# Performance work log

Measured on AMD Instinct MI355X. Metric: run time of the kernel, lower is better.

Reference implementation:

```python
import jax, jax.numpy as jnp
import numpy as np
import math

B, N, C, H = 32, 512, 768, 12
HD = C // H
KEEP_RATE = 0.7
SCALE = HD ** -0.5
BOUNDARY = math.ceil(KEEP_RATE * (N - 1))  # 358


def setup_inputs() -> dict:
    key = jax.random.key(0)
    k1, k2, k3, k4 = jax.random.split(key, 4)
    x = jax.random.normal(k1, (B, N, C), jnp.float32) * 0.02
    # prefix (left-aligned) key-padding mask: valid length per sample in [N//4, N]
    lengths = jax.random.randint(k2, (B,), N // 4, N + 1)
    key_mask = (jnp.arange(N)[None, :] < lengths[:, None])  # [B, N]
    attn_mask = jnp.broadcast_to(key_mask[:, None, :], (B, N, N)).astype(jnp.int32)
    w_qkv = jax.random.normal(k3, (C, 3 * C), jnp.float32) * (C ** -0.5)
    w_proj = jax.random.normal(k4, (C, C), jnp.float32) * (C ** -0.5)
    b_proj = jnp.zeros((C,), jnp.float32)
    return {"x": x, "attn_mask": attn_mask, "w_qkv": w_qkv, "w_proj": w_proj, "b_proj": b_proj}


def reference(x, attn_mask, w_qkv, w_proj, b_proj):
    # qkv projection and head split: [B,N,3C] -> [3,B,H,N,HD]
    qkv = (x @ w_qkv).reshape(B, N, 3, H, HD).transpose(2, 0, 3, 1, 4)
    q, k, v = qkv[0], qkv[1], qkv[2]
    attn = jnp.einsum('bhqd,bhkd->bhqk', q, k) * SCALE          # [B,H,N,N]
    mask4 = attn_mask[:, None, :, :]                            # broadcast over heads
    attn = jnp.where(mask4 == 0, jnp.float32(-1e9), attn)
    attn = jax.nn.softmax(attn, axis=-1)
    out = jnp.einsum('bhqk,bhkd->bhqd', attn, v)                # [B,H,N,HD]
    out = out.transpose(0, 2, 1, 3).reshape(B, N, C)
    out = out @ w_proj + b_proj

    # per-sample top-k token pruning based on CLS attention (keep_rate < 1)
    key_row = attn_mask[:, 0, 1:]                               # [B, N-1] key padding row
    cls_mean = attn[:, :, 0, 1:].mean(axis=1)                   # mean over heads, [B, N-1]
    valid = key_row != 0
    scores = jnp.where(valid, cls_mean, -jnp.inf)
    valid_count = valid.sum(axis=1)                             # [B]
    left = jnp.ceil(valid_count.astype(jnp.float32) * KEEP_RATE).astype(jnp.int32)
    _, top_idx = jax.lax.top_k(scores, BOUNDARY)                # sorted desc, [B, BOUNDARY]
    pos = jnp.arange(BOUNDARY)[None, :]
    # slots beyond per-sample left_tokens are padded with 1e9 (matches torch cat padding)
    idx = jnp.where(pos < left[:, None], top_idx.astype(jnp.float32), jnp.float32(1e9))
    index = jnp.broadcast_to(idx[:, :, None], (B, BOUNDARY, C))
    return (out, index, idx, BOUNDARY)
```

## Files before the change

### kernel.cpp

```cpp
#include <hip/hip_runtime.h>
#include <hip/hip_bf16.h>

#define Bb 32
#define Nn 512
#define Cc 768
#define Hh 12
#define HDd 64
#define BND 358
#define QS 0.18033688f

typedef unsigned short u16;
typedef unsigned int u32;
typedef __attribute__((ext_vector_type(8))) short bf16x8;
typedef __attribute__((ext_vector_type(4))) float f32x4;
typedef __attribute__((ext_vector_type(16))) float f32x16;
typedef __attribute__((ext_vector_type(4))) int i32x4;

__device__ __forceinline__ f32x4 MFMA16(bf16x8 a, bf16x8 b, f32x4 c) {
  return __builtin_amdgcn_mfma_f32_16x16x32_bf16(a, b, c, 0, 0, 0);
}
__device__ __forceinline__ f32x16 MFMA32(bf16x8 a, bf16x8 b, f32x16 c) {
  return __builtin_amdgcn_mfma_f32_32x32x16_bf16(a, b, c, 0, 0, 0);
}

__device__ __forceinline__ float fexp2(float x) { return __builtin_amdgcn_exp2f(x); }

__device__ __forceinline__ u32 f2bf(float f) {
  u32 u = __builtin_bit_cast(u32, f);
  return (u + 0x7fffu + ((u >> 16) & 1u)) >> 16;
}
__device__ __forceinline__ u32 packbf2(float a, float b) { return f2bf(a) | (f2bf(b) << 16); }
__device__ __forceinline__ u32 cvtpk2(float a, float b) {
  float2 f2 = {a, b};
  __hip_bfloat162 h = __float22bfloat162_rn(f2);
  u32 r;
  __builtin_memcpy(&r, &h, 4);
  return r;
}
__device__ __forceinline__ float bf2f(u16 h) { return __builtin_bit_cast(float, (u32)h << 16); }

__device__ __forceinline__ void async_copy16(void* lds, const void* g) {
  __builtin_amdgcn_global_load_lds((const __attribute__((address_space(1))) void*)g,
                                   (__attribute__((address_space(3))) void*)lds, 16, 0, 0);
}


__global__ __launch_bounds__(256) void k_convx(const float* __restrict__ x, u16* __restrict__ xb) {
  int gid = blockIdx.x * 256 + threadIdx.x;
  if (gid >= (Bb * Nn * Cc) / 4) return;
  float4 v = *(const float4*)&x[gid * 4];
  u32 p0 = packbf2(v.x, v.y), p1 = packbf2(v.z, v.w);
  uint2 st = {p0, p1};
  *(uint2*)&xb[gid * 4] = st;
}

__global__ __launch_bounds__(256) void k_transpose(const float* __restrict__ src, u16* __restrict__ dst,
                                                   int R, int Ccols) {
  __shared__ float tbuf[32][33];
  int c0 = blockIdx.x * 32, r0 = blockIdx.y * 32;
  int lx = threadIdx.x & 31, ly = threadIdx.x >> 5;
  #pragma unroll
  for (int rr = ly; rr < 32; rr += 8) tbuf[rr][lx] = src[(long)(r0 + rr) * Ccols + c0 + lx];
  __syncthreads();
  #pragma unroll
  for (int cc = ly; cc < 32; cc += 8) dst[(long)(c0 + cc) * R + r0 + lx] = (u16)f2bf(tbuf[lx][cc]);
}

__global__ __launch_bounds__(256) void k_lens(const int* __restrict__ mask, int* __restrict__ lens) {
  int b = blockIdx.x, t = threadIdx.x;
  __shared__ int red[256];
  red[t] = mask[(long)b * Nn * Nn + t] + mask[(long)b * Nn * Nn + t + 256];
  __syncthreads();
  for (int s = 128; s > 0; s >>= 1) {
    if (t < s) red[t] += red[t + s];
    __syncthreads();
  }
  if (t == 0) lens[b] = red[0];
}

__global__ __launch_bounds__(64) void k_order(const int* __restrict__ lens, int* __restrict__ ord) {
  __shared__ int ls[32];
  int t = threadIdx.x;
  if (t < 32) ls[t] = lens[t];
  __syncthreads();
  if (t < 32) {
    int mylen = ls[t];
    int rank = 0;
    #pragma unroll
    for (int j = 0; j < 32; ++j) {
      int lj = ls[j];
      rank += (lj > mylen || (lj == mylen && j < t)) ? 1 : 0;
    }
    int s = (rank < 16) ? (2 * rank) : (2 * (31 - rank) + 1);
    ord[s] = t;
  }
}

template <int MODE, int SWAP>
__global__ __launch_bounds__(256) void k_gemm2(const u16* __restrict__ A, const u16* __restrict__ Bt,
                                               int nb0, u16* __restrict__ Qo, u16* __restrict__ Ko,
                                               u16* __restrict__ Vto, float* __restrict__ Co,
                                               const float* __restrict__ bias) {
  __shared__ u16 As[2][128 * 64];
  __shared__ u16 Bs[2][128 * 64];
  int m0 = blockIdx.x * 128;
  int nb = nb0 + blockIdx.y * 128;
  int t = threadIdx.x, lane = t & 63, wave = t >> 6;
  int wr = wave >> 1, wc = wave & 1;
  int qlane = lane & 15, g = lane >> 4;
  f32x4 acc[4][4] = {};

  auto stage = [&](int kt, int buf) {
    #pragma unroll
    for (int i = 0; i < 4; ++i) {
      int chunk = i * 256 + t;
      int row = chunk >> 3;
      int cp = (chunk & 7) << 4;
      int src = cp ^ ((row & 7) << 4);
      const u16* ga = A + (long)(m0 + row) * 768 + kt * 64 + (src >> 1);
      const u16* gb = Bt + (long)(nb + row) * 768 + kt * 64 + (src >> 1);
      async_copy16(&As[buf][(i * 256 + wave * 64) * 8], ga);
      async_copy16(&Bs[buf][(i * 256 + wave * 64) * 8], gb);
    }
  };

  auto compute = [&](int buf) {
    #pragma unroll
    for (int kk = 0; kk < 2; ++kk) {
      bf16x8 af[4], bf[4];
      #pragma unroll
      for (int x = 0; x < 4; ++x) {
        int ra = wr * 64 + x * 16 + qlane;
        int ca = (kk * 64 + g * 16) ^ ((ra & 7) << 4);
        af[x] = *(const bf16x8*)&As[buf][ra * 64 + (ca >> 1)];
        int rb = wc * 64 + x * 16 + qlane;
        int cb = (kk * 64 + g * 16) ^ ((rb & 7) << 4);
        bf[x] = *(const bf16x8*)&Bs[buf][rb * 64 + (cb >> 1)];
      }
      #pragma unroll
      for (int mi = 0; mi < 4; ++mi)
        #pragma unroll
        for (int ni = 0; ni < 4; ++ni)
          acc[mi][ni] = SWAP ? MFMA16(bf[ni], af[mi], acc[mi][ni])
                             : MFMA16(af[mi], bf[ni], acc[mi][ni]);
    }
  };

  stage(0, 0);
  __syncthreads();
  int cur = 0;
  for (int kt = 0; kt < 12; ++kt) {
    if (kt < 11) stage(kt + 1, cur ^ 1);
    compute(cur);
    __syncthreads();
    cur ^= 1;
  }

  if (MODE == 0 && SWAP == 1) {
    #pragma unroll
    for (int mi = 0; mi < 4; ++mi) {
      int m = m0 + wr * 64 + mi * 16 + qlane;
      int b = m >> 9, qi = m & 511;
      #pragma unroll
      for (int ni = 0; ni < 4; ++ni) {
        int nf = nb + wc * 64 + ni * 16 + g * 4;
        int which = nf >= 768;
        int rem = nf - which * 768;
        int hh = rem >> 6, d0 = rem & 63;
        u16* dst = (which ? Ko : Qo) + ((long)(b * Hh + hh) * Nn + qi) * HDd + d0;
        float sc = which ? 1.f : QS;
        uint2 st = {packbf2(acc[mi][ni][0] * sc, acc[mi][ni][1] * sc),
                    packbf2(acc[mi][ni][2] * sc, acc[mi][ni][3] * sc)};
        *(uint2*)dst = st;
      }
    }
  } else if (MODE == 0) {
    #pragma unroll
    for (int mi = 0; mi < 4; ++mi) {
      int m = m0 + wr * 64 + mi * 16 + g * 4;
      int b = m >> 9, qi = m & 511;
      #pragma unroll
      for (int ni = 0; ni < 4; ++ni) {
        int rem = nb + wc * 64 + ni * 16 + qlane - 1536;
        int hh = rem >> 6, d = rem & 63;
        u16* dst = Vto + (long)(b * Hh + hh) * (Nn * HDd) + (qi >> 5) * 2048 + d * 32 + (qi & 31);
        uint2 st = {packbf2(acc[mi][ni][0], acc[mi][ni][1]),
                    packbf2(acc[mi][ni][2], acc[mi][ni][3])};
        *(uint2*)dst = st;
      }
    }
  } else {
    #pragma unroll
    for (int mi = 0; mi < 4; ++mi) {
      #pragma unroll
      for (int ni = 0; ni < 4; ++ni) {
        int n = nb + wc * 64 + ni * 16 + qlane;
        float bv = bias[n];
        #pragma unroll
        for (int r = 0; r < 4; ++r) {
          int m = m0 + wr * 64 + mi * 16 + g * 4 + r;
          Co[(long)m * Cc + n] = acc[mi][ni][r] + bv;
        }
      }
    }
  }
}

__global__ __launch_bounds__(64) void k_attn(const u16* __restrict__ Q, const u16* __restrict__ K,
                                             const u16* __restrict__ Vt, const int* __restrict__ lens,
                                             const int* __restrict__ ord, u16* __restrict__ AO) {
  int lane = threadIdx.x;
  int bid = blockIdx.x;
  int bh = bid % (Bb * Hh);
  int chunk = bid / (Bb * Hh);
  int b = ord[bh / Hh];
  int h = bh % Hh;
  int q0w = chunk * 64;
  int ln = lane & 31, hi = lane >> 5;
  int len = lens[b];
  int nt = (len + 31) >> 5;

  const u16* Qb = Q + (long)(b * Hh + h) * Nn * HDd;
  const u16* Kb = K + (long)(b * Hh + h) * Nn * HDd;
  const u16* Vb = Vt + (long)(b * Hh + h) * Nn * HDd;

  bf16x8 qf[2][4];
  #pragma unroll
  for (int qt = 0; qt < 2; ++qt)
    #pragma unroll
    for (int ds = 0; ds < 4; ++ds)
      qf[qt][ds] = *(const bf16x8*)(Qb + (q0w + qt * 32 + ln) * HDd + ds * 16 + hi * 8);

  f32x16 o[2][2] = {};
  float l[2] = {0.f, 0.f};

  auto loadt = [&](bf16x8 (&kf)[4], bf16x8 (&vf)[2][2], int t) {
    int k0 = t * 32;
    #pragma unroll
    for (int ds = 0; ds < 4; ++ds)
      kf[ds] = *(const bf16x8*)(Kb + (k0 + ln) * HDd + ds * 16 + hi * 8);
    #pragma unroll
    for (int dt = 0; dt < 2; ++dt)
      #pragma unroll
      for (int ks = 0; ks < 2; ++ks)
        vf[dt][ks] = *(const bf16x8*)(Vb + t * 2048 + (dt * 32 + ln) * 32 + ks * 16 + hi * 8);
  };

  auto compute = [&](const bf16x8 (&kf)[4], const bf16x8 (&vf)[2][2], int t) {
    int k0 = t * 32;
    bool bdry = (k0 + 32 > len);
    int khi = k0 + 4 * hi;
    #pragma unroll
    for (int qt = 0; qt < 2; ++qt) {
      f32x16 st = {};
      #pragma unroll
      for (int ds = 0; ds < 4; ++ds) st = MFMA32(kf[ds], qf[qt][ds], st);
      if (bdry) {
        #pragma unroll
        for (int r = 0; r < 16; ++r) {
          int key = khi + (r & 3) + 8 * (r >> 2);
          if (key >= len) st[r] = -1e9f;
        }
      }
      float p[16];
      #pragma unroll
      for (int r = 0; r < 16; ++r) p[r] = fexp2(st[r]);
      l[qt] += (((p[0] + p[1]) + (p[2] + p[3])) + ((p[4] + p[5]) + (p[6] + p[7]))) +
               (((p[8] + p[9]) + (p[10] + p[11])) + ((p[12] + p[13]) + (p[14] + p[15])));
      u32 wA0 = cvtpk2(p[0], p[1]), wA1 = cvtpk2(p[2], p[3]);
      u32 wA2 = cvtpk2(p[4], p[5]), wA3 = cvtpk2(p[6], p[7]);
      asm volatile("v_permlane32_swap_b32 %0, %1" : "+v"(wA0), "+v"(wA2));
      asm volatile("v_permlane32_swap_b32 %0, %1" : "+v"(wA1), "+v"(wA3));
      u32 wB0 = cvtpk2(p[8], p[9]), wB1 = cvtpk2(p[10], p[11]);
      u32 wB2 = cvtpk2(p[12], p[13]), wB3 = cvtpk2(p[14], p[15]);
      asm volatile("v_permlane32_swap_b32 %0, %1" : "+v"(wB0), "+v"(wB2));
      asm volatile("v_permlane32_swap_b32 %0, %1" : "+v"(wB1), "+v"(wB3));
      i32x4 bi0 = {(int)wA0, (int)wA1, (int)wA2, (int)wA3};
      i32x4 bi1 = {(int)wB0, (int)wB1, (int)wB2, (int)wB3};
      bf16x8 pb0 = __builtin_bit_cast(bf16x8, bi0);
      bf16x8 pb1 = __builtin_bit_cast(bf16x8, bi1);
      #pragma unroll
      for (int dt = 0; dt < 2; ++dt) {
        o[qt][dt] = MFMA32(vf[dt][0], pb0, o[qt][dt]);
        o[qt][dt] = MFMA32(vf[dt][1], pb1, o[qt][dt]);
      }
    }
  };

  bf16x8 kfA[4], vfA[2][2], kfB[4], vfB[2][2];
  loadt(kfA, vfA, 0);
  int t = 0;
  #pragma unroll 1
  for (; t + 2 <= nt; t += 2) {
    loadt(kfB, vfB, t + 1);
    compute(kfA, vfA, t);
    if (t + 2 < nt) loadt(kfA, vfA, t + 2);
    compute(kfB, vfB, t + 1);
  }
  if (t < nt) compute(kfA, vfA, t);

  #pragma unroll
  for (int qt = 0; qt < 2; ++qt) {
    float ls = l[qt] + __shfl_xor(l[qt], 32);
    float inv = 1.f / ls;
    u16* outp = AO + ((long)(b * Nn + q0w + qt * 32 + ln) * Cc) + h * HDd;
    #pragma unroll
    for (int dt = 0; dt < 2; ++dt) {
      #pragma unroll
      for (int qd = 0; qd < 4; ++qd) {
        uint2 st2 = {cvtpk2(o[qt][dt][4 * qd + 0] * inv, o[qt][dt][4 * qd + 1] * inv),
                     cvtpk2(o[qt][dt][4 * qd + 2] * inv, o[qt][dt][4 * qd + 3] * inv)};
        *(uint2*)(outp + dt * 32 + 8 * qd + 4 * hi) = st2;
      }
    }
  }
}

__global__ __launch_bounds__(256) void k_sco_init(float* __restrict__ sco) {
  int gid = blockIdx.x * 256 + threadIdx.x;
  if (gid < Bb * 511) sco[gid] = 0.f;
}

__global__ __launch_bounds__(256) void k_cls(const u16* __restrict__ Q, const u16* __restrict__ K,
                                             const int* __restrict__ lens, float* __restrict__ scores) {
  int bh = blockIdx.x;
  int b = bh / Hh;
  int t = threadIdx.x;
  int len = lens[b];
  __shared__ float qrow[64];
  __shared__ float red[256];
  const u16* Qb = Q + (long)bh * Nn * HDd;
  const u16* Kb = K + (long)bh * Nn * HDd;
  if (t < 64) qrow[t] = bf2f(Qb[t]);
  __syncthreads();
  const bf16x8* kr0 = (const bf16x8*)(Kb + t * HDd);
  const bf16x8* kr1 = (const bf16x8*)(Kb + (t + 256) * HDd);
  float d0 = 0.f, d1 = 0.f;
  #pragma unroll
  for (int c8 = 0; c8 < 8; ++c8) {
    bf16x8 kv0 = kr0[c8], kv1 = kr1[c8];
    #pragma unroll
    for (int j = 0; j < 8; ++j) {
      float qv = qrow[c8 * 8 + j];
      d0 += qv * bf2f((u16)kv0[j]);
      d1 += qv * bf2f((u16)kv1[j]);
    }
  }
  float l0 = (t < len) ? d0 : -1e9f;
  float l1 = (t + 256 < len) ? d1 : -1e9f;
  red[t] = fmaxf(l0, l1);
  __syncthreads();
  for (int ss = 128; ss > 0; ss >>= 1) {
    if (t < ss) red[t] = fmaxf(red[t], red[t + ss]);
    __syncthreads();
  }
  float mx = red[0];
  __syncthreads();
  float e0 = fexp2(l0 - mx), e1 = fexp2(l1 - mx);
  red[t] = e0 + e1;
  __syncthreads();
  for (int ss = 128; ss > 0; ss >>= 1) {
    if (t < ss) red[t] += red[t + ss];
    __syncthreads();
  }
  float w = (1.f / 12.f) / red[0];
  if (t >= 1) atomicAdd(&scores[b * 511 + (t - 1)], e0 * w);
  atomicAdd(&scores[b * 511 + (t + 255)], e1 * w);
}

__device__ __forceinline__ bool sless(float sa, int ia, float sb, int ib) {
  return (sa > sb) || (sa == sb && ia < ib);
}

__global__ __launch_bounds__(256) void k_topk(const float* __restrict__ scores,
                                              const int* __restrict__ lens, float* __restrict__ dout) {
  int b = blockIdx.x, t = threadIdx.x;
  __shared__ float sc[512];
  __shared__ int id[512];
  float ninf = -__builtin_inff();
  int len = lens[b];
  for (int i = t; i < 512; i += 256) {
    sc[i] = (i < 511 && (i + 1) < len) ? scores[b * 511 + i] : ninf;
    id[i] = i;
  }
  for (int k = 2; k <= 512; k <<= 1) {
    for (int j = k >> 1; j > 0; j >>= 1) {
      __syncthreads();
      for (int i = t; i < 512; i += 256) {
        int ixj = i ^ j;
        if (ixj > i) {
          float si = sc[i], sj = sc[ixj];
          int ii = id[i], ij = id[ixj];
          bool up = ((i & k) == 0);
          bool dosw = up ? sless(sj, ij, si, ii) : sless(si, ii, sj, ij);
          if (dosw) {
            sc[i] = sj; sc[ixj] = si;
            id[i] = ij; id[ixj] = ii;
          }
        }
      }
    }
  }
  __syncthreads();
  int left = (int)ceilf((float)(len - 1) * 0.7f);
  const long OFF_IDX = (long)Bb * Nn * Cc + (long)Bb * BND * Cc;
  for (int p = t; p < BND; p += 256) {
    dout[OFF_IDX + (long)b * BND + p] = (p < left) ? (float)id[p] : 1e9f;
  }
  if (b == 0 && t == 0) dout[OFF_IDX + (long)Bb * BND] = (float)BND;
}

__global__ __launch_bounds__(256) void k_bcast(float* __restrict__ dout) {
  long gid = (long)blockIdx.x * 256 + threadIdx.x;
  const long total = (long)Bb * BND * (Cc / 4);
  if (gid >= total) return;
  long bp = gid / (Cc / 4);
  int c4 = (int)(gid % (Cc / 4));
  const long OFF_INDEX = (long)Bb * Nn * Cc;
  const long OFF_IDX = OFF_INDEX + (long)Bb * BND * Cc;
  float v = dout[OFF_IDX + bp];
  float4 f = {v, v, v, v};
  *(float4*)&dout[OFF_INDEX + bp * Cc + (long)c4 * 4] = f;
}

extern "C" void kernel_launch(void* const* d_in, const int* in_sizes, int n_in,
                              void* d_out, int out_size, void* d_ws, size_t ws_size,
                              hipStream_t stream) {
  const float* x = (const float*)d_in[0];
  const int* mask = (const int*)d_in[1];
  const float* wqkv = (const float*)d_in[2];
  const float* wproj = (const float*)d_in[3];
  const float* bproj = (const float*)d_in[4];
  float* out = (float*)d_out;

  char* ws = (char*)d_ws;
  u16* Qw  = (u16*)(ws);
  u16* Kw  = (u16*)(ws + 25165824L);
  u16* Vtw = (u16*)(ws + 50331648L);
  u16* XB  = (u16*)(ws + 75497472L);
  u16* AO  = XB;
  u16* WQT = (u16*)(ws + 100663296L);
  u16* WPT = (u16*)(ws + 104202240L);
  float* SCO = (float*)(ws + 105381888L);
  int* LEN = (int*)(ws + 105447424L);
  int* ORD = (int*)(ws + 105447552L);

  k_convx<<<12288, 256, 0, stream>>>(x, XB);
  k_transpose<<<dim3(72, 24), 256, 0, stream>>>(wqkv, WQT, 768, 2304);
  k_transpose<<<dim3(24, 24), 256, 0, stream>>>(wproj, WPT, 768, 768);
  k_lens<<<32, 256, 0, stream>>>(mask, LEN);
  k_order<<<1, 64, 0, stream>>>(LEN, ORD);
  k_sco_init<<<64, 256, 0, stream>>>(SCO);
  k_gemm2<0, 1><<<dim3(128, 12), 256, 0, stream>>>(XB, WQT, 0, Qw, Kw, nullptr, nullptr, nullptr);
  k_gemm2<0, 0><<<dim3(128, 6), 256, 0, stream>>>(XB, WQT, 1536, nullptr, nullptr, Vtw, nullptr, nullptr);
  k_attn<<<3072, 64, 0, stream>>>(Qw, Kw, Vtw, LEN, ORD, AO);
  k_gemm2<1, 0><<<dim3(128, 6), 256, 0, stream>>>(AO, WPT, 0, nullptr, nullptr, nullptr, out, bproj);
  k_cls<<<384, 256, 0, stream>>>(Qw, Kw, LEN, SCO);
  k_topk<<<32, 256, 0, stream>>>(SCO, LEN, out);
  k_bcast<<<8592, 256, 0, stream>>>(out);
}
```

Before: 217.5 us.

## Merge QKV GEMM launches, single-buffer LDS, reorder attention blocks, add MFMA priority

Folds the QK and V projection GEMMs into one launch, choosing the swapped MFMA operand order at runtime from blockIdx.y. The GEMM drops LDS double buffering for a single buffer with a sync before and after each k-tile, which halves shared memory and may raise occupancy but exposes load latency. The attention kernel now maps blocks batch-fastest (b from bh&31, h from bh>>5) so concurrently running blocks span different sequence lengths. It also wraps the MFMA groups in s_setprio to favour matrix issue.

```diff
diff --git a/kernel.cpp b/kernel.cpp
--- a/kernel.cpp
+++ b/kernel.cpp
@@ -96,21 +96,22 @@
   }
 }
 
-template <int MODE, int SWAP>
+template <int MODE>
 __global__ __launch_bounds__(256) void k_gemm2(const u16* __restrict__ A, const u16* __restrict__ Bt,
-                                               int nb0, u16* __restrict__ Qo, u16* __restrict__ Ko,
+                                               u16* __restrict__ Qo, u16* __restrict__ Ko,
                                                u16* __restrict__ Vto, float* __restrict__ Co,
                                                const float* __restrict__ bias) {
-  __shared__ u16 As[2][128 * 64];
-  __shared__ u16 Bs[2][128 * 64];
+  __shared__ u16 As[128 * 64];
+  __shared__ u16 Bs[128 * 64];
   int m0 = blockIdx.x * 128;
-  int nb = nb0 + blockIdx.y * 128;
+  int nb = blockIdx.y * 128;
+  bool sw = (MODE == 0) && (blockIdx.y < 12);
   int t = threadIdx.x, lane = t & 63, wave = t >> 6;
   int wr = wave >> 1, wc = wave & 1;
   int qlane = lane & 15, g = lane >> 4;
   f32x4 acc[4][4] = {};
 
-  auto stage = [&](int kt, int buf) {
+  for (int kt = 0; kt < 12; ++kt) {
     #pragma unroll
     for (int i = 0; i < 4; ++i) {
       int chunk = i * 256 + t;
@@ -119,12 +120,10 @@
       int src = cp ^ ((row & 7) << 4);
       const u16* ga = A + (long)(m0 + row) * 768 + kt * 64 + (src >> 1);
       const u16* gb = Bt + (long)(nb + row) * 768 + kt * 64 + (src >> 1);
-      async_copy16(&As[buf][(i * 256 + wave * 64) * 8], ga);
-      async_copy16(&Bs[buf][(i * 256 + wave * 64) * 8], gb);
-    }
-  };
-
-  auto compute = [&](int buf) {
+      async_copy16(&As[(i * 256 + wave * 64) * 8], ga);
+      async_copy16(&Bs[(i * 256 + wave * 64) * 8], gb);
+    }
+    __syncthreads();
     #pragma unroll
     for (int kk = 0; kk < 2; ++kk) {
       bf16x8 af[4], bf[4];
@@ -132,31 +131,27 @@
       for (int x = 0; x < 4; ++x) {
         int ra = wr * 64 + x * 16 + qlane;
         int ca = (kk * 64 + g * 16) ^ ((ra & 7) << 4);
-        af[x] = *(const bf16x8*)&As[buf][ra * 64 + (ca >> 1)];
+        af[x] = *(const bf16x8*)&As[ra * 64 + (ca >> 1)];
         int rb = wc * 64 + x * 16 + qlane;
         int cb = (kk * 64 + g * 16) ^ ((rb & 7) << 4);
-        bf[x] = *(const bf16x8*)&Bs[buf][rb * 64 + (cb >> 1)];
-      }
-      #pragma unroll
-      for (int mi = 0; mi < 4; ++mi)
+        bf[x] = *(const bf16x8*)&Bs[rb * 64 + (cb >> 1)];
+      }
+      if (sw) {
         #pragma unroll
-        for (int ni = 0; ni < 4; ++ni)
-          acc[mi][ni] = SWAP ? MFMA16(bf[ni], af[mi], acc[mi][ni])
-                             : MFMA16(af[mi], bf[ni], acc[mi][ni]);
-    }
-  };
-
-  stage(0, 0);
-  __syncthreads();
-  int cur = 0;
-  for (int kt = 0; kt < 12; ++kt) {
-    if (kt < 11) stage(kt + 1, cur ^ 1);
-    compute(cur);
+        for (int mi = 0; mi < 4; ++mi)
+          #pragma unroll
+          for (int ni = 0; ni < 4; ++ni) acc[mi][ni] = MFMA16(bf[ni], af[mi], acc[mi][ni]);
+      } else {
+        #pragma unroll
+        for (int mi = 0; mi < 4; ++mi)
+          #pragma unroll
+          for (int ni = 0; ni < 4; ++ni) acc[mi][ni] = MFMA16(af[mi], bf[ni], acc[mi][ni]);
+      }
+    }
     __syncthreads();
-    cur ^= 1;
-  }
-
-  if (MODE == 0 && SWAP == 1) {
+  }
+
+  if (MODE == 0 && blockIdx.y < 12) {
     #pragma unroll
     for (int mi = 0; mi < 4; ++mi) {
       int m = m0 + wr * 64 + mi * 16 + qlane;
@@ -213,8 +208,8 @@
   int bid = blockIdx.x;
   int bh = bid % (Bb * Hh);
   int chunk = bid / (Bb * Hh);
-  int b = ord[bh / Hh];
-  int h = bh % Hh;
+  int b = ord[bh & 31];
+  int h = bh >> 5;
   int q0w = chunk * 64;
   int ln = lane & 31, hi = lane >> 5;
   int len = lens[b];
@@ -253,8 +248,10 @@
     #pragma unroll
     for (int qt = 0; qt < 2; ++qt) {
       f32x16 st = {};
+      __builtin_amdgcn_s_setprio(1);
       #pragma unroll
       for (int ds = 0; ds < 4; ++ds) st = MFMA32(kf[ds], qf[qt][ds], st);
+      __builtin_amdgcn_s_setprio(0);
       if (bdry) {
         #pragma unroll
         for (int r = 0; r < 16; ++r) {
@@ -279,11 +276,13 @@
       i32x4 bi1 = {(int)wB0, (int)wB1, (int)wB2, (int)wB3};
       bf16x8 pb0 = __builtin_bit_cast(bf16x8, bi0);
       bf16x8 pb1 = __builtin_bit_cast(bf16x8, bi1);
+      __builtin_amdgcn_s_setprio(1);
       #pragma unroll
       for (int dt = 0; dt < 2; ++dt) {
         o[qt][dt] = MFMA32(vf[dt][0], pb0, o[qt][dt]);
         o[qt][dt] = MFMA32(vf[dt][1], pb1, o[qt][dt]);
       }
+      __builtin_amdgcn_s_setprio(0);
     }
   };
 
@@ -451,10 +450,9 @@
   k_lens<<<32, 256, 0, stream>>>(mask, LEN);
   k_order<<<1, 64, 0, stream>>>(LEN, ORD);
   k_sco_init<<<64, 256, 0, stream>>>(SCO);
-  k_gemm2<0, 1><<<dim3(128, 12), 256, 0, stream>>>(XB, WQT, 0, Qw, Kw, nullptr, nullptr, nullptr);
-  k_gemm2<0, 0><<<dim3(128, 6), 256, 0, stream>>>(XB, WQT, 1536, nullptr, nullptr, Vtw, nullptr, nullptr);
+  k_gemm2<0><<<dim3(128, 18), 256, 0, stream>>>(XB, WQT, Qw, Kw, Vtw, nullptr, nullptr);
   k_attn<<<3072, 64, 0, stream>>>(Qw, Kw, Vtw, LEN, ORD, AO);
-  k_gemm2<1, 0><<<dim3(128, 6), 256, 0, stream>>>(AO, WPT, 0, nullptr, nullptr, nullptr, out, bproj);
+  k_gemm2<1><<<dim3(128, 6), 256, 0, stream>>>(AO, WPT, nullptr, nullptr, nullptr, out, bproj);
   k_cls<<<384, 256, 0, stream>>>(Qw, Kw, LEN, SCO);
   k_topk<<<32, 256, 0, stream>>>(SCO, LEN, out);
   k_bcast<<<8592, 256, 0, stream>>>(out);
```

After: 243.0 us. +11.8%, slower.
